# Performance work log

Hardware: AMD Instinct MI355X
Metric: run time of the kernel (lower is better)

## Reference

```python
import jax, jax.numpy as jnp
import numpy as np

EPS_SLOPE = 1e-4
EPS_AVG = 1e-8
MIN_AVG = 1e-6
EPS_SCALE = 1e-3


def _slopes_yk(xk, delta_raw):
    # xk: [D, K] sorted knot x-positions; delta_raw: [D, K-1]
    seg_dx = xk[:, 1:] - xk[:, :-1]                      # [D, K-1]
    slopes = jax.nn.softplus(delta_raw) + EPS_SLOPE       # [D, K-1]
    avg = (slopes * seg_dx).sum(1, keepdims=True) / (seg_dx.sum(1, keepdims=True) + EPS_AVG)
    avg = jnp.maximum(avg, MIN_AVG)
    slopes = slopes / avg
    yk = jnp.concatenate(
        [jnp.zeros((xk.shape[0], 1), dtype=xk.dtype), jnp.cumsum(slopes * seg_dx, axis=1)],
        axis=1,
    )                                                     # [D, K]
    return slopes, yk


def setup_inputs() -> dict:
    key = jax.random.key(0)
    k1, k2, k3, k4, k5 = jax.random.split(key, 5)
    N, D, K = 1_000_000, 64, 32
    x = jax.random.normal(k1, (N, D), dtype=jnp.float32)
    # sorted knots per dim, spanning roughly the data range
    xk = jnp.sort(jax.random.normal(k2, (D, K), dtype=jnp.float32) * 2.0, axis=1)
    delta_raw = jax.random.normal(k3, (D, K - 1), dtype=jnp.float32) * 0.1
    scale_raw = jax.random.normal(k4, (D,), dtype=jnp.float32) * 0.1
    shift = jax.random.normal(k5, (D,), dtype=jnp.float32) * 0.1
    return {"x": x, "xk": xk, "delta_raw": delta_raw, "scale_raw": scale_raw, "shift": shift}


def reference(x, xk, delta_raw, scale_raw, shift):
    # x: [N, D]; xk: [D, K]
    D, K = xk.shape
    slopes, yk = _slopes_yk(xk, delta_raw)
    xT = x.T                                              # [D, N]
    # per-dim binary search (torch.searchsorted default == side='left')
    idx = jax.vmap(lambda knots, vals: jnp.searchsorted(knots, vals))(xk, xT)
    i0 = jnp.clip(idx, 1, K - 1) - 1                      # [D, N]
    x0 = jnp.take_along_axis(xk, i0, axis=1)              # [D, N]
    y0 = jnp.take_along_axis(yk, i0, axis=1)
    m = jnp.take_along_axis(slopes, i0, axis=1)
    y = (y0 + m * (xT - x0)).T                            # [N, D]
    scale = jax.nn.softplus(scale_raw) + EPS_SCALE
    return y * scale + shift
```

## Files before the change

### kernel.cpp

```cpp
#include <hip/hip_runtime.h>
#include <math.h>

#define D 64
#define KNOTS 32
#define NSEG 31
#define G 512
#define TSTR 66

typedef float f2v __attribute__((ext_vector_type(2)));

__device__ __forceinline__ float softplus_f(float v) {
  return fmaxf(v, 0.f) + log1pf(expf(-fabsf(v)));
}

__global__ __launch_bounds__(1024, 8) void pwl_fused(
    const float* __restrict__ x, const float* __restrict__ xk,
    const float* __restrict__ delta_raw, const float* __restrict__ scale_raw,
    const float* __restrict__ shift, float* __restrict__ out, int nrows) {
  __shared__ float kL[KNOTS * D];
  __shared__ float2 sAB[NSEG * D];
  __shared__ unsigned char tab[G * TSTR];
  __shared__ float invS[D], nloS[D];

  const int tid = threadIdx.x;

  for (int i = tid; i < D * KNOTS; i += blockDim.x) {
    int d = i >> 5, j = i & 31;
    int sd = (d >> 1) | ((d & 1) << 5);
    kL[j * D + sd] = xk[i];
  }
  __syncthreads();

  if (tid < D) {
    const int sd = tid;
    const int d = ((sd & 31) << 1) | (sd >> 5);
    float num = 0.f, den = 0.f;
    for (int s = 0; s < NSEG; ++s) {
      float sp = softplus_f(delta_raw[d * NSEG + s]) + 1e-4f;
      float dx = kL[(s + 1) * D + sd] - kL[s * D + sd];
      num += sp * dx;
      den += dx;
    }
    float avg = fmaxf(num / (den + 1e-8f), 1e-6f);
    float scale = softplus_f(scale_raw[d]) + 1e-3f;
    float sh = shift[d];
    float y = 0.f;
    for (int s = 0; s < NSEG; ++s) {
      float sp = softplus_f(delta_raw[d * NSEG + s]) + 1e-4f;
      float m = sp / avg;
      float k0 = kL[s * D + sd];
      sAB[s * D + sd] = make_float2(m * scale, (y - m * k0) * scale + sh);
      y += m * (kL[(s + 1) * D + sd] - k0);
    }
    float lo = kL[1 * D + sd];
    float hi = kL[(KNOTS - 1) * D + sd];
    float inv = (float)G / (hi - lo);
    invS[sd] = inv;
    nloS[sd] = -lo * inv;
  }
  __syncthreads();

  for (int p = tid; p < G * D; p += blockDim.x) {
    const int sd = p & 63;
    const int c = p >> 6;
    const float inv = invS[sd], nlo = nloS[sd];
    int b = 0;
#pragma unroll
    for (int half = 16; half > 0; half >>= 1) {
      float kv = kL[(b + half) * D + sd];
      float cf = fminf(fmaxf(fmaf(kv, inv, nlo), 0.f), (float)(G - 1));
      b += ((int)cf < c) ? half : 0;
    }
    tab[c * TSTR + sd] = (unsigned char)min(b, 30);
  }
  __syncthreads();

  const int lane = tid & 63;
  const int m = lane & 31;
  const int sd0 = m;
  const int sd1 = 32 + m;
  const float inv0 = invS[sd0], nlo0 = nloS[sd0];
  const float inv1 = invS[sd1], nlo1 = nloS[sd1];

  const f2v* __restrict__ x2 = (const f2v*)x;
  f2v* __restrict__ o2 = (f2v*)out;

  auto evalpair = [&](f2v xv) -> f2v {
    float cf0 = fminf(fmaxf(fmaf(xv.x, inv0, nlo0), 0.f), (float)(G - 1));
    float cf1 = fminf(fmaxf(fmaf(xv.y, inv1, nlo1), 0.f), (float)(G - 1));
    int c0 = (int)cf0, c1 = (int)cf1;
    int i0 = tab[c0 * TSTR + sd0];
    int i1 = tab[c1 * TSTR + sd1];
    float2 a0 = sAB[i0 * D + sd0];
    float2 a1 = sAB[i1 * D + sd1];
    f2v r;
    r.x = fmaf(a0.x, xv.x, a0.y);
    r.y = fmaf(a1.x, xv.y, a1.y);
    return r;
  };

  const int gwave = (int)(blockIdx.x * blockDim.x + tid) >> 6;
  const int nwave = (int)(gridDim.x * blockDim.x) >> 6;
  const int ngroups = nrows >> 4;
  const int chunk = (ngroups + nwave - 1) / nwave;
  int g = gwave * chunk;
  const int gend = min(g + chunk, ngroups);

  f2v a0, a1, a2, a3, a4, a5, a6, a7;
  f2v b0, b1, b2, b3, b4, b5, b6, b7;

#define LOADG(p, gg)                                                   \
  {                                                                    \
    const int base_ = (gg) * 512 + lane;                               \
    p##0 = x2[base_];        p##1 = x2[base_ + 64];                    \
    p##2 = x2[base_ + 128];  p##3 = x2[base_ + 192];                   \
    p##4 = x2[base_ + 256];  p##5 = x2[base_ + 320];                   \
    p##6 = x2[base_ + 384];  p##7 = x2[base_ + 448];                   \
  }

#define PROCG(p, gg)                                                   \
  {                                                                    \
    const int base_ = (gg) * 512 + lane;                               \
    f2v r_;                                                            \
    r_ = evalpair(p##0); __builtin_nontemporal_store(r_, &o2[base_]);       \
    r_ = evalpair(p##1); __builtin_nontemporal_store(r_, &o2[base_ + 64]);  \
    r_ = evalpair(p##2); __builtin_nontemporal_store(r_, &o2[base_ + 128]); \
    r_ = evalpair(p##3); __builtin_nontemporal_store(r_, &o2[base_ + 192]); \
    r_ = evalpair(p##4); __builtin_nontemporal_store(r_, &o2[base_ + 256]); \
    r_ = evalpair(p##5); __builtin_nontemporal_store(r_, &o2[base_ + 320]); \
    r_ = evalpair(p##6); __builtin_nontemporal_store(r_, &o2[base_ + 384]); \
    r_ = evalpair(p##7); __builtin_nontemporal_store(r_, &o2[base_ + 448]); \
  }

  if (g < gend) {
    LOADG(a, g);
    while (true) {
      const int gn = g + 1;
      if (gn < gend) {
        LOADG(b, gn);
        PROCG(a, g);
        const int gnn = gn + 1;
        if (gnn < gend) {
          LOADG(a, gnn);
          PROCG(b, gn);
          g = gnn;
        } else {
          PROCG(b, gn);
          break;
        }
      } else {
        PROCG(a, g);
        break;
      }
    }
  }
#undef LOADG
#undef PROCG

  const int tg0 = ngroups << 4;
  for (int r = tg0 + gwave; r < nrows; r += nwave) {
    if (lane < 32) {
      const int bi = r * 32 + m;
      f2v xv = x2[bi];
      f2v rv = evalpair(xv);
      __builtin_nontemporal_store(rv, &o2[bi]);
    }
  }
}

extern "C" void kernel_launch(void* const* d_in, const int* in_sizes, int n_in,
                              void* d_out, int out_size, void* d_ws, size_t ws_size,
                              hipStream_t stream) {
  const float* x = (const float*)d_in[0];
  const float* xk = (const float*)d_in[1];
  const float* delta_raw = (const float*)d_in[2];
  const float* scale_raw = (const float*)d_in[3];
  const float* shift = (const float*)d_in[4];
  float* out = (float*)d_out;

  const int nrows = in_sizes[0] / D;
  const int block = 1024;
  const int grid = 512;
  pwl_fused<<<grid, block, 0, stream>>>(x, xk, delta_raw, scale_raw, shift,
                                        out, nrows);
}
```

Baseline: 112.7 us.

## Widen global accesses to float4 and transpose LUT tables to per-dim rows

Switches global loads and stores from 2-float to 4-float vectors, so each lane now handles four dimensions (q, q+16, q+32, q+48), and the dimension swizzle is changed to match. The bucket table and the slope/intercept tables are moved to a dimension-major layout with padding (TPAD 516, SPAD 33), and the packed float2 coefficients are split into separate sA/sB arrays. The aim is fewer, wider memory instructions per row and different LDS bank behaviour for the data-dependent lookups. In exchange, each lane issues more scattered LDS reads, and the dimension-major layout may cause more bank conflicts because the lookup indices depend on the data.

```diff
diff --git a/kernel.cpp b/kernel.cpp
--- a/kernel.cpp
+++ b/kernel.cpp
@@ -5,9 +5,10 @@
 #define KNOTS 32
 #define NSEG 31
 #define G 512
-#define TSTR 66
+#define TPAD 516
+#define SPAD 33
 
-typedef float f2v __attribute__((ext_vector_type(2)));
+typedef float f4v __attribute__((ext_vector_type(4)));
 
 __device__ __forceinline__ float softplus_f(float v) {
   return fmaxf(v, 0.f) + log1pf(expf(-fabsf(v)));
@@ -18,22 +19,23 @@
     const float* __restrict__ delta_raw, const float* __restrict__ scale_raw,
     const float* __restrict__ shift, float* __restrict__ out, int nrows) {
   __shared__ float kL[KNOTS * D];
-  __shared__ float2 sAB[NSEG * D];
-  __shared__ unsigned char tab[G * TSTR];
+  __shared__ float sA[D * SPAD];
+  __shared__ float sB[D * SPAD];
+  __shared__ unsigned char tab[D * TPAD];
   __shared__ float invS[D], nloS[D];
 
   const int tid = threadIdx.x;
 
   for (int i = tid; i < D * KNOTS; i += blockDim.x) {
     int d = i >> 5, j = i & 31;
-    int sd = (d >> 1) | ((d & 1) << 5);
+    int sd = (d >> 2) | ((d & 3) << 4);
     kL[j * D + sd] = xk[i];
   }
   __syncthreads();
 
   if (tid < D) {
     const int sd = tid;
-    const int d = ((sd & 31) << 1) | (sd >> 5);
+    const int d = ((sd & 15) << 2) | (sd >> 4);
     float num = 0.f, den = 0.f;
     for (int s = 0; s < NSEG; ++s) {
       float sp = softplus_f(delta_raw[d * NSEG + s]) + 1e-4f;
@@ -49,7 +51,8 @@
       float sp = softplus_f(delta_raw[d * NSEG + s]) + 1e-4f;
       float m = sp / avg;
       float k0 = kL[s * D + sd];
-      sAB[s * D + sd] = make_float2(m * scale, (y - m * k0) * scale + sh);
+      sA[sd * SPAD + s] = m * scale;
+      sB[sd * SPAD + s] = (y - m * k0) * scale + sh;
       y += m * (kL[(s + 1) * D + sd] - k0);
     }
     float lo = kL[1 * D + sd];
@@ -71,31 +74,35 @@
       float cf = fminf(fmaxf(fmaf(kv, inv, nlo), 0.f), (float)(G - 1));
       b += ((int)cf < c) ? half : 0;
     }
-    tab[c * TSTR + sd] = (unsigned char)min(b, 30);
+    tab[sd * TPAD + c] = (unsigned char)min(b, 30);
   }
   __syncthreads();
 
   const int lane = tid & 63;
-  const int m = lane & 31;
-  const int sd0 = m;
-  const int sd1 = 32 + m;
+  const int q = lane & 15;
+  const int sd0 = q, sd1 = q + 16, sd2 = q + 32, sd3 = q + 48;
   const float inv0 = invS[sd0], nlo0 = nloS[sd0];
   const float inv1 = invS[sd1], nlo1 = nloS[sd1];
+  const float inv2 = invS[sd2], nlo2 = nloS[sd2];
+  const float inv3 = invS[sd3], nlo3 = nloS[sd3];
 
-  const f2v* __restrict__ x2 = (const f2v*)x;
-  f2v* __restrict__ o2 = (f2v*)out;
+  const f4v* __restrict__ x4 = (const f4v*)x;
+  f4v* __restrict__ o4 = (f4v*)out;
 
-  auto evalpair = [&](f2v xv) -> f2v {
+  auto evalquad = [&](f4v xv) -> f4v {
     float cf0 = fminf(fmaxf(fmaf(xv.x, inv0, nlo0), 0.f), (float)(G - 1));
     float cf1 = fminf(fmaxf(fmaf(xv.y, inv1, nlo1), 0.f), (float)(G - 1));
-    int c0 = (int)cf0, c1 = (int)cf1;
-    int i0 = tab[c0 * TSTR + sd0];
-    int i1 = tab[c1 * TSTR + sd1];
-    float2 a0 = sAB[i0 * D + sd0];
-    float2 a1 = sAB[i1 * D + sd1];
-    f2v r;
-    r.x = fmaf(a0.x, xv.x, a0.y);
-    r.y = fmaf(a1.x, xv.y, a1.y);
+    float cf2 = fminf(fmaxf(fmaf(xv.z, inv2, nlo2), 0.f), (float)(G - 1));
+    float cf3 = fminf(fmaxf(fmaf(xv.w, inv3, nlo3), 0.f), (float)(G - 1));
+    int i0 = tab[sd0 * TPAD + (int)cf0];
+    int i1 = tab[sd1 * TPAD + (int)cf1];
+    int i2 = tab[sd2 * TPAD + (int)cf2];
+    int i3 = tab[sd3 * TPAD + (int)cf3];
+    f4v r;
+    r.x = fmaf(sA[sd0 * SPAD + i0], xv.x, sB[sd0 * SPAD + i0]);
+    r.y = fmaf(sA[sd1 * SPAD + i1], xv.y, sB[sd1 * SPAD + i1]);
+    r.z = fmaf(sA[sd2 * SPAD + i2], xv.z, sB[sd2 * SPAD + i2]);
+    r.w = fmaf(sA[sd3 * SPAD + i3], xv.w, sB[sd3 * SPAD + i3]);
     return r;
   };
 
@@ -106,30 +113,24 @@
   int g = gwave * chunk;
   const int gend = min(g + chunk, ngroups);
 
-  f2v a0, a1, a2, a3, a4, a5, a6, a7;
-  f2v b0, b1, b2, b3, b4, b5, b6, b7;
+  f4v a0, a1, a2, a3;
+  f4v b0, b1, b2, b3;
 
-#define LOADG(p, gg)                                                   \
-  {                                                                    \
-    const int base_ = (gg) * 512 + lane;                               \
-    p##0 = x2[base_];        p##1 = x2[base_ + 64];                    \
-    p##2 = x2[base_ + 128];  p##3 = x2[base_ + 192];                   \
-    p##4 = x2[base_ + 256];  p##5 = x2[base_ + 320];                   \
-    p##6 = x2[base_ + 384];  p##7 = x2[base_ + 448];                   \
+#define LOADG(p, gg)                                      \
+  {                                                       \
+    const int base_ = (gg) * 256 + lane;                  \
+    p##0 = x4[base_];        p##1 = x4[base_ + 64];       \
+    p##2 = x4[base_ + 128];  p##3 = x4[base_ + 192];      \
   }
 
-#define PROCG(p, gg)                                                   \
-  {                                                                    \
-    const int base_ = (gg) * 512 + lane;                               \
-    f2v r_;                                                            \
-    r_ = evalpair(p##0); __builtin_nontemporal_store(r_, &o2[base_]);       \
-    r_ = evalpair(p##1); __builtin_nontemporal_store(r_, &o2[base_ + 64]);  \
-    r_ = evalpair(p##2); __builtin_nontemporal_store(r_, &o2[base_ + 128]); \
-    r_ = evalpair(p##3); __builtin_nontemporal_store(r_, &o2[base_ + 192]); \
-    r_ = evalpair(p##4); __builtin_nontemporal_store(r_, &o2[base_ + 256]); \
-    r_ = evalpair(p##5); __builtin_nontemporal_store(r_, &o2[base_ + 320]); \
-    r_ = evalpair(p##6); __builtin_nontemporal_store(r_, &o2[base_ + 384]); \
-    r_ = evalpair(p##7); __builtin_nontemporal_store(r_, &o2[base_ + 448]); \
+#define PROCG(p, gg)                                                        \
+  {                                                                         \
+    const int base_ = (gg) * 256 + lane;                                    \
+    f4v r_;                                                                 \
+    r_ = evalquad(p##0); __builtin_nontemporal_store(r_, &o4[base_]);       \
+    r_ = evalquad(p##1); __builtin_nontemporal_store(r_, &o4[base_ + 64]);  \
+    r_ = evalquad(p##2); __builtin_nontemporal_store(r_, &o4[base_ + 128]); \
+    r_ = evalquad(p##3); __builtin_nontemporal_store(r_, &o4[base_ + 192]); \
   }
 
   if (g < gend) {
@@ -157,13 +158,13 @@
 #undef LOADG
 #undef PROCG
 
-  const int tg0 = ngroups << 4;
-  for (int r = tg0 + gwave; r < nrows; r += nwave) {
-    if (lane < 32) {
-      const int bi = r * 32 + m;
-      f2v xv = x2[bi];
-      f2v rv = evalpair(xv);
-      __builtin_nontemporal_store(rv, &o2[bi]);
+  const int tr0 = ngroups << 4;
+  for (int r = tr0 + gwave; r < nrows; r += nwave) {
+    if (lane < 16) {
+      const int bi = r * 16 + q;
+      f4v xv = x4[bi];
+      f4v rv = evalquad(xv);
+      __builtin_nontemporal_store(rv, &o4[bi]);
     }
   }
 }
```

Result: no change. 113.8 us (+0.9%).
